# Kernel tuning notes

Hardware: AMD Instinct MI355X
Metric: run time of the kernel (lower is better)

Reference implementation:

```python
import jax, jax.numpy as jnp
import numpy as np

# Standard SMPL kinematic tree (24 joints); parents[0] = -1 (root)
PARENTS = np.array([-1, 0, 0, 0, 1, 2, 3, 4, 5, 6, 7, 8, 9, 9, 9, 12, 13, 14, 16, 17, 18, 19, 20, 21], dtype=np.int32)
B, V, J, NSHAPE, NPOSEBASIS = 512, 6890, 24, 10, 207


def setup_inputs() -> dict:
    key = jax.random.key(0)
    ks = jax.random.split(key, 9)
    poses = jax.random.normal(ks[0], (B, J * 3), dtype=jnp.float32) * 0.2
    shapes = jax.random.normal(ks[1], (B, NSHAPE), dtype=jnp.float32)
    Rh = jax.random.normal(ks[2], (B, 3), dtype=jnp.float32) * 0.2
    Th = jax.random.normal(ks[3], (B, 3), dtype=jnp.float32)
    v_template = jax.random.normal(ks[4], (V, 3), dtype=jnp.float32)
    shapedirs = jax.random.normal(ks[5], (V, 3, NSHAPE), dtype=jnp.float32) * 0.01
    posedirs = jax.random.normal(ks[6], (NPOSEBASIS, V * 3), dtype=jnp.float32) * 0.01
    jr = jax.random.uniform(ks[7], (J, V), dtype=jnp.float32)
    J_regressor = jr / jnp.sum(jr, axis=1, keepdims=True)
    w = jax.random.uniform(ks[8], (V, J), dtype=jnp.float32)
    weights = w / jnp.sum(w, axis=1, keepdims=True)
    return {"poses": poses, "shapes": shapes, "Rh": Rh, "Th": Th,
            "v_template": v_template, "shapedirs": shapedirs, "posedirs": posedirs,
            "J_regressor": J_regressor, "weights": weights}


def batch_rodrigues(rot_vecs):
    # rot_vecs: (N,3) -> (N,3,3); matches smplx batch_rodrigues
    angle = jnp.linalg.norm(rot_vecs + 1e-8, axis=1, keepdims=True)  # (N,1)
    rd = rot_vecs / angle
    cos = jnp.cos(angle)[:, :, None]
    sin = jnp.sin(angle)[:, :, None]
    rx, ry, rz = rd[:, 0], rd[:, 1], rd[:, 2]
    zeros = jnp.zeros_like(rx)
    K = jnp.stack([zeros, -rz, ry, rz, zeros, -rx, -ry, rx, zeros], axis=1).reshape(-1, 3, 3)
    ident = jnp.eye(3, dtype=rot_vecs.dtype)[None]
    return ident + sin * K + (1.0 - cos) * jnp.matmul(K, K)


def smpl_forward(poses, shapes, Rh, Th, v_template, shapedirs, posedirs, J_regressor, weights):
    bn = poses.shape[0]
    # shape blendshapes: v_shaped (B,V,3)
    v_shaped = v_template[None] + jnp.einsum('bl,vdl->bvd', shapes, shapedirs)
    # rest-pose joints (B,J,3)
    Jrest = jnp.einsum('jv,bvd->bjd', J_regressor, v_shaped)
    # per-joint rotation matrices
    rot_mats = batch_rodrigues(poses.reshape(-1, 3)).reshape(bn, J, 3, 3)
    # pose blendshapes
    ident = jnp.eye(3, dtype=poses.dtype)
    pose_feature = (rot_mats[:, 1:] - ident).reshape(bn, -1)  # (B,207)
    v_posed = v_shaped + jnp.matmul(pose_feature, posedirs).reshape(bn, V, 3)
    # kinematic chain rigid transforms
    rel_joints = jnp.concatenate([Jrest[:, :1], Jrest[:, 1:] - Jrest[:, PARENTS[1:]]], axis=1)
    bottom = jnp.tile(jnp.array([0., 0., 0., 1.], dtype=poses.dtype), (bn, J, 1, 1))
    tmats = jnp.concatenate([jnp.concatenate([rot_mats, rel_joints[..., None]], axis=-1), bottom], axis=-2)  # (B,J,4,4)
    chain = [tmats[:, 0]]
    for i in range(1, J):
        chain.append(jnp.matmul(chain[PARENTS[i]], tmats[:, i]))
    transforms = jnp.stack(chain, axis=1)  # (B,J,4,4)
    # remove rest-pose joint location from transforms
    tj = jnp.einsum('bjik,bjk->bji', transforms[:, :, :3, :3], Jrest)
    A = transforms.at[:, :, :3, 3].add(-tj)
    # linear blend skinning
    T = jnp.einsum('vj,bjik->bvik', weights, A)  # (B,V,4,4)
    verts = jnp.einsum('bvik,bvk->bvi', T[:, :, :3, :3], v_posed) + T[:, :, :3, 3]
    # global rotation + translation
    rot = batch_rodrigues(Rh)  # (B,3,3)
    vertices = jnp.einsum('bij,bvj->bvi', rot, verts) + Th[:, None]
    return vertices


def reference(poses, shapes, Rh, Th, v_template, shapedirs, posedirs, J_regressor, weights):
    return smpl_forward(poses, shapes, Rh, Th, v_template, shapedirs, posedirs, J_regressor, weights)
```

## Files before the change

kernel.cpp:

```cpp
#include <hip/hip_runtime.h>


#define BN 512
#define NV 6890
#define NVP 6912
#define NJ 24
#define NS 10
#define NP 207
#define PSTR 208
#define KP 224
#define K2 32
#define NPAD 20736
#define BB 8
#define TV 256

#define WS_JSP 0
#define WS_G   6400
#define WS_PF  153856
#define WS_A1  12800
#define WS_A2  127488
#define WS_WT  324096
#define WS_BT  545280
#define FULL_NEED ((size_t)10380288)
#define FB_NEED   ((size_t)1041408)

typedef unsigned short u16;
typedef short bf16x8 __attribute__((ext_vector_type(8)));
typedef float f32x4  __attribute__((ext_vector_type(4)));

__constant__ int c_par[NJ] = {-1,0,0,0,1,2,3,4,5,6,7,8,9,9,9,12,13,14,16,17,18,19,20,21};

__device__ __forceinline__ u16 f2bf(float f){
    union { float f; unsigned i; } x; x.f = f;
    unsigned r = x.i + 0x7fffu + ((x.i >> 16) & 1u);
    return (u16)(r >> 16);
}

__global__ __launch_bounds__(256) void k_jreg(const float* __restrict__ jreg,
                                              const float* __restrict__ vt,
                                              const float* __restrict__ sd,
                                              float* __restrict__ ws){
    int j = blockIdx.x, s = blockIdx.y;
    int tid = threadIdx.x;
    int v0 = s*864, v1 = min(NV, v0+864);
    float acc[33];
    #pragma unroll
    for(int k=0;k<33;k++) acc[k]=0.f;
    for(int v=v0+tid; v<v1; v+=256){
        float jr = jreg[j*NV+v];
        #pragma unroll
        for(int d=0;d<3;d++) acc[d] = fmaf(jr, vt[v*3+d], acc[d]);
        const float2* sp = (const float2*)(sd + (size_t)v*30);
        #pragma unroll
        for(int k=0;k<15;k++){
            float2 s2 = sp[k];
            acc[3+2*k]   = fmaf(jr, s2.x, acc[3+2*k]);
            acc[3+2*k+1] = fmaf(jr, s2.y, acc[3+2*k+1]);
        }
    }
    __shared__ float red[4][33];
    int lane = tid & 63, wv = tid >> 6;
    #pragma unroll
    for(int k=0;k<33;k++){
        float val = acc[k];
        #pragma unroll
        for(int off=32; off; off>>=1) val += __shfl_down(val, off, 64);
        if(lane==0) red[wv][k]=val;
    }
    __syncthreads();
    if(tid<33) ws[WS_JSP + (j*8+s)*33 + tid] = red[0][tid]+red[1][tid]+red[2][tid]+red[3][tid];
}

__global__ __launch_bounds__(256) void k_conv(const float* __restrict__ pd,
                                              const float* __restrict__ sd,
                                              u16* __restrict__ bt){
    __shared__ u16 tile[32][65];
    int t = threadIdx.x;
    int n0 = blockIdx.x * 64;
    int k0 = blockIdx.y * 32;
    int nl = t & 63, kb = (t>>6)*8;
    int n = n0 + nl;
    #pragma unroll
    for(int i=0;i<8;i++){
        int k = k0 + kb + i;
        float v = 0.f;
        if(n < NV*3){
            if(k < NP)           v = pd[(size_t)k*(NV*3) + n];
            else if(k < NP+NS)   v = sd[(size_t)(n/3)*30 + (n%3)*10 + (k-NP)];
        }
        tile[kb+i][nl] = f2bf(v);
    }
    __syncthreads();
    int nl2 = t >> 2, kc = t & 3;
    union { u16 s[8]; uint4 q; } u;
    #pragma unroll
    for(int i=0;i<8;i++) u.s[i] = tile[kc*8+i][nl2];
    int ng = n0 + nl2;
    int row = (ng%3)*NVP + ng/3;
    u16* dst = bt + (size_t)row*KP + k0 + kc*8;
    *(uint4*)dst = u.q;
}

__global__ __launch_bounds__(256) void k_wconv(const float* __restrict__ wts,
                                               u16* __restrict__ wt){
    int v = blockIdx.x*256 + threadIdx.x;
    if(v >= NVP) return;
    union { u16 s[32]; uint4 q[4]; } u;
    #pragma unroll
    for(int j=0;j<24;j++) u.s[j] = (v<NV) ? f2bf(wts[(size_t)v*24+j]) : (u16)0;
    #pragma unroll
    for(int j=24;j<32;j++) u.s[j]=0;
    uint4* dst = (uint4*)(wt + (size_t)v*K2);
    dst[0]=u.q[0]; dst[1]=u.q[1]; dst[2]=u.q[2]; dst[3]=u.q[3];
}

__global__ __launch_bounds__(64) void k_chain(const float* __restrict__ poses,
                                              const float* __restrict__ shapes,
                                              const float* __restrict__ Rh,
                                              float* __restrict__ ws,
                                              u16* __restrict__ a1,
                                              u16* __restrict__ a2,
                                              int full){
    int b = blockIdx.x;
    int t = threadIdx.x;
    __shared__ float R[25][9];
    __shared__ float sh[NS];
    __shared__ float js[792];
    __shared__ float jrest[NJ][3];
    __shared__ float rel[NJ][3];
    __shared__ float chR[NJ][9];
    __shared__ float chT[NJ][3];
    __shared__ float Gs[NJ][12];

    if(t<25){
        float x,y,z;
        if(t<24){ x=poses[b*72+t*3]; y=poses[b*72+t*3+1]; z=poses[b*72+t*3+2]; }
        else    { x=Rh[b*3];         y=Rh[b*3+1];         z=Rh[b*3+2]; }
        float ax=x+1e-8f, ay=y+1e-8f, az=z+1e-8f;
        float ang = sqrtf(ax*ax+ay*ay+az*az);
        float inv = 1.f/ang;
        float rx=x*inv, ry=y*inv, rz=z*inv;
        float s = sinf(ang), c = cosf(ang), oc = 1.f - c;
        R[t][0]=1.f+oc*(-rz*rz-ry*ry); R[t][1]=-s*rz+oc*(rx*ry);      R[t][2]= s*ry+oc*(rx*rz);
        R[t][3]= s*rz+oc*(rx*ry);      R[t][4]=1.f+oc*(-rz*rz-rx*rx); R[t][5]=-s*rx+oc*(ry*rz);
        R[t][6]=-s*ry+oc*(rx*rz);      R[t][7]= s*rx+oc*(ry*rz);      R[t][8]=1.f+oc*(-ry*ry-rx*rx);
    }
    if(t<NS) sh[t]=shapes[b*NS+t];
    for(int idx=t; idx<792; idx+=64){
        int j = idx/33, e = idx%33;
        float a = 0.f;
        #pragma unroll
        for(int s=0;s<8;s++) a += ws[WS_JSP + (j*8+s)*33 + e];
        js[idx]=a;
    }
    __syncthreads();

    for(int idx=t; idx<KP; idx+=64){
        float v = 0.f;
        if(idx<NP){
            int j = 1 + idx/9, e = idx%9;
            v = R[j][e] - ((e==0||e==4||e==8)?1.f:0.f);
        } else if(idx<NP+NS) v = sh[idx-NP];
        if(full){ a1[b*KP + idx] = f2bf(v); }
        else if(idx<PSTR) ws[WS_PF + b*PSTR + idx] = (idx<NP)?v:0.f;
    }
    if(t<NJ){
        #pragma unroll
        for(int d=0;d<3;d++){
            float a = js[t*33 + d];
            #pragma unroll
            for(int l=0;l<NS;l++) a = fmaf(sh[l], js[t*33 + 3 + d*10 + l], a);
            jrest[t][d]=a;
        }
    }
    __syncthreads();
    if(t<NJ){
        int p = c_par[t];
        #pragma unroll
        for(int d=0;d<3;d++) rel[t][d] = (t==0) ? jrest[0][d] : jrest[t][d]-jrest[p][d];
    }
    __syncthreads();
    if(t<9) chR[0][t]=R[0][t];
    if(t<3) chT[0][t]=rel[0][t];
    __syncthreads();
    for(int i=1;i<NJ;i++){
        if(t<12){
            int r=t>>2, cc=t&3, p=c_par[i];
            if(cc<3){
                chR[i][r*3+cc] = chR[p][r*3+0]*R[i][0*3+cc] + chR[p][r*3+1]*R[i][1*3+cc] + chR[p][r*3+2]*R[i][2*3+cc];
            } else {
                chT[i][r] = chR[p][r*3+0]*rel[i][0] + chR[p][r*3+1]*rel[i][1] + chR[p][r*3+2]*rel[i][2] + chT[p][r];
            }
        }
        __syncthreads();
    }
    if(t<NJ){
        float rg[9];
        #pragma unroll
        for(int k=0;k<9;k++) rg[k]=R[24][k];
        float at[3];
        #pragma unroll
        for(int r=0;r<3;r++){
            float tj = chR[t][r*3+0]*jrest[t][0] + chR[t][r*3+1]*jrest[t][1] + chR[t][r*3+2]*jrest[t][2];
            at[r] = chT[t][r] - tj;
        }
        #pragma unroll
        for(int r=0;r<3;r++){
            #pragma unroll
            for(int cc=0;cc<3;cc++)
                Gs[t][r*4+cc] = rg[r*3+0]*chR[t][0*3+cc] + rg[r*3+1]*chR[t][1*3+cc] + rg[r*3+2]*chR[t][2*3+cc];
            Gs[t][r*4+3] = rg[r*3+0]*at[0] + rg[r*3+1]*at[1] + rg[r*3+2]*at[2];
        }
    }
    __syncthreads();
    if(full){
        for(int idx=t; idx<12*K2; idx+=64){
            int e = idx/K2, k = idx%K2;
            float v = (k<NJ) ? Gs[k][e] : 0.f;
            a2[((size_t)e*BN + b)*K2 + k] = f2bf(v);
        }
    } else if(t<NJ){
        float* g = &ws[WS_G + b*288 + t*12];
        #pragma unroll
        for(int e=0;e<12;e++) g[e] = Gs[t][e];
    }
}

__global__ __launch_bounds__(256) void k_fused(const u16* __restrict__ A1,
                                               const u16* __restrict__ A2,
                                               const u16* __restrict__ WT,
                                               const u16* __restrict__ BT,
                                               const float* __restrict__ vt,
                                               const float* __restrict__ th,
                                               float* __restrict__ out){
    int t = threadIdx.x;
    int wave = t>>6, lane = t&63;
    int quad = lane>>4, l16 = lane&15;
    int m0 = blockIdx.x*32 + (wave&1)*16;
    int v0 = blockIdx.y*32 + (wave>>1)*16;
    f32x4 zz = {0.f,0.f,0.f,0.f};
    f32x4 accP[3]; accP[0]=zz; accP[1]=zz; accP[2]=zz;
    f32x4 accT[12];
    #pragma unroll
    for(int e=0;e<12;e++) accT[e]=zz;

    const u16* a1 = A1 + (size_t)(m0 + l16)*KP + quad*8;
    const u16* b0 = BT + ((size_t)0*NVP + v0 + l16)*KP + quad*8;
    const u16* b1 = BT + ((size_t)1*NVP + v0 + l16)*KP + quad*8;
    const u16* b2 = BT + ((size_t)2*NVP + v0 + l16)*KP + quad*8;
    #pragma unroll
    for(int k0=0;k0<KP;k0+=32){
        bf16x8 af = *(const bf16x8*)(a1 + k0);
        bf16x8 f0 = *(const bf16x8*)(b0 + k0);
        bf16x8 f1 = *(const bf16x8*)(b1 + k0);
        bf16x8 f2 = *(const bf16x8*)(b2 + k0);
        accP[0] = __builtin_amdgcn_mfma_f32_16x16x32_bf16(af, f0, accP[0], 0,0,0);
        accP[1] = __builtin_amdgcn_mfma_f32_16x16x32_bf16(af, f1, accP[1], 0,0,0);
        accP[2] = __builtin_amdgcn_mfma_f32_16x16x32_bf16(af, f2, accP[2], 0,0,0);
    }
    bf16x8 wf = *(const bf16x8*)(WT + (size_t)(v0 + l16)*K2 + quad*8);
    #pragma unroll
    for(int e=0;e<12;e++){
        bf16x8 gf = *(const bf16x8*)(A2 + ((size_t)e*BN + m0 + l16)*K2 + quad*8);
        accT[e] = __builtin_amdgcn_mfma_f32_16x16x32_bf16(gf, wf, accT[e], 0,0,0);
    }
    int v = v0 + l16;
    if(v < NV){
        float vt0 = vt[v*3], vt1 = vt[v*3+1], vt2 = vt[v*3+2];
        #pragma unroll
        for(int r=0;r<4;r++){
            int b = m0 + quad*4 + r;
            float p0 = accP[0][r] + vt0;
            float p1 = accP[1][r] + vt1;
            float p2 = accP[2][r] + vt2;
            float o0 = fmaf(accT[0][r],p0, fmaf(accT[1][r],p1, fmaf(accT[2][r], p2, accT[3][r]))) + th[b*3+0];
            float o1 = fmaf(accT[4][r],p0, fmaf(accT[5][r],p1, fmaf(accT[6][r], p2, accT[7][r]))) + th[b*3+1];
            float o2 = fmaf(accT[8][r],p0, fmaf(accT[9][r],p1, fmaf(accT[10][r],p2, accT[11][r]))) + th[b*3+2];
            float* op = out + ((size_t)b*NV + v)*3;
            op[0]=o0; op[1]=o1; op[2]=o2;
        }
    }
}

__global__ __launch_bounds__(256) void k_main(const float* __restrict__ vt,
                                              const float* __restrict__ sd,
                                              const float* __restrict__ pd,
                                              const float* __restrict__ wts,
                                              const float* __restrict__ th,
                                              const float* __restrict__ shapes,
                                              const float* __restrict__ ws,
                                              float* __restrict__ out){
    __shared__ __align__(16) float pf_s[BB*PSTR];
    __shared__ __align__(16) float g_s[BB*288];
    __shared__ float th_s[BB*3];
    __shared__ float sh_s[BB*NS];
    int tid = threadIdx.x;
    int b0  = blockIdx.y * BB;
    int v   = blockIdx.x * TV + tid;

    for(int i=tid; i<BB*PSTR; i+=TV) pf_s[i] = ws[WS_PF + b0*PSTR + i];
    for(int i=tid; i<BB*288;  i+=TV) g_s[i]  = ws[WS_G  + b0*288  + i];
    if(tid<BB*3)  th_s[tid] = th[b0*3+tid];
    if(tid<BB*NS) sh_s[tid] = shapes[b0*NS+tid];
    __syncthreads();
    if(v>=NV) return;

    float sdv[30];
    {
        const float2* sp = (const float2*)(sd + (size_t)v*30);
        #pragma unroll
        for(int i=0;i<15;i++){ float2 s2 = sp[i]; sdv[2*i]=s2.x; sdv[2*i+1]=s2.y; }
    }
    float vt0=vt[v*3], vt1=vt[v*3+1], vt2=vt[v*3+2];
    float vp[BB][3];
    #pragma unroll
    for(int b=0;b<BB;b++){
        #pragma unroll
        for(int d=0;d<3;d++){
            float a = (d==0)?vt0:((d==1)?vt1:vt2);
            #pragma unroll
            for(int l=0;l<NS;l++) a = fmaf(sh_s[b*NS+l], sdv[d*10+l], a);
            vp[b][d]=a;
        }
    }
    const float* pcol = pd + (size_t)v*3;
    int p=0;
    for(; p<=NP-4; p+=4){
        float pdv[4][3];
        #pragma unroll
        for(int q=0;q<4;q++){
            size_t base = (size_t)(p+q)*(NV*3);
            pdv[q][0]=pcol[base]; pdv[q][1]=pcol[base+1]; pdv[q][2]=pcol[base+2];
        }
        #pragma unroll
        for(int b=0;b<BB;b++){
            float4 f = *(const float4*)&pf_s[b*PSTR+p];
            #pragma unroll
            for(int d=0;d<3;d++)
                vp[b][d] = fmaf(f.x,pdv[0][d], fmaf(f.y,pdv[1][d], fmaf(f.z,pdv[2][d], fmaf(f.w,pdv[3][d], vp[b][d]))));
        }
    }
    for(; p<NP; p++){
        size_t base=(size_t)p*(NV*3);
        float p0=pcol[base], p1=pcol[base+1], p2=pcol[base+2];
        #pragma unroll
        for(int b=0;b<BB;b++){
            float f = pf_s[b*PSTR+p];
            vp[b][0]=fmaf(f,p0,vp[b][0]); vp[b][1]=fmaf(f,p1,vp[b][1]); vp[b][2]=fmaf(f,p2,vp[b][2]);
        }
    }
    float w[24];
    {
        const float4* wp = (const float4*)(wts + (size_t)v*24);
        #pragma unroll
        for(int i=0;i<6;i++){
            float4 u = wp[i];
            w[i*4+0]=u.x; w[i*4+1]=u.y; w[i*4+2]=u.z; w[i*4+3]=u.w;
        }
    }
    #pragma unroll 1
    for(int b=0;b<BB;b++){
        float4 T0=make_float4(0.f,0.f,0.f,0.f), T1=T0, T2=T0;
        #pragma unroll
        for(int j=0;j<NJ;j++){
            float wj = w[j];
            const float4* g = (const float4*)&g_s[b*288 + j*12];
            float4 g0=g[0], g1=g[1], g2=g[2];
            T0.x=fmaf(wj,g0.x,T0.x); T0.y=fmaf(wj,g0.y,T0.y); T0.z=fmaf(wj,g0.z,T0.z); T0.w=fmaf(wj,g0.w,T0.w);
            T1.x=fmaf(wj,g1.x,T1.x); T1.y=fmaf(wj,g1.y,T1.y); T1.z=fmaf(wj,g1.z,T1.z); T1.w=fmaf(wj,g1.w,T1.w);
            T2.x=fmaf(wj,g2.x,T2.x); T2.y=fmaf(wj,g2.y,T2.y); T2.z=fmaf(wj,g2.z,T2.z); T2.w=fmaf(wj,g2.w,T2.w);
        }
        float x=vp[b][0], y=vp[b][1], z=vp[b][2];
        float ox = fmaf(T0.x,x, fmaf(T0.y,y, fmaf(T0.z,z, T0.w))) + th_s[b*3+0];
        float oy = fmaf(T1.x,x, fmaf(T1.y,y, fmaf(T1.z,z, T1.w))) + th_s[b*3+1];
        float oz = fmaf(T2.x,x, fmaf(T2.y,y, fmaf(T2.z,z, T2.w))) + th_s[b*3+2];
        size_t o = ((size_t)(b0+b)*NV + v)*3;
        out[o]=ox; out[o+1]=oy; out[o+2]=oz;
    }
}

extern "C" void kernel_launch(void* const* d_in, const int* in_sizes, int n_in,
                              void* d_out, int out_size, void* d_ws, size_t ws_size,
                              hipStream_t stream){
    const float* poses  = (const float*)d_in[0];
    const float* shapes = (const float*)d_in[1];
    const float* Rh     = (const float*)d_in[2];
    const float* Th     = (const float*)d_in[3];
    const float* vt     = (const float*)d_in[4];
    const float* sd     = (const float*)d_in[5];
    const float* pdirs  = (const float*)d_in[6];
    const float* jreg   = (const float*)d_in[7];
    const float* wts    = (const float*)d_in[8];
    float* ws  = (float*)d_ws;
    float* out = (float*)d_out;
    u16* u = (u16*)d_ws;
    int full = (ws_size >= FULL_NEED) ? 1 : 0;

    hipLaunchKernelGGL(k_jreg, dim3(NJ,8), dim3(256), 0, stream, jreg, vt, sd, ws);
    hipLaunchKernelGGL(k_chain, dim3(BN), dim3(64), 0, stream, poses, shapes, Rh, ws,
                       u + WS_A1, u + WS_A2, full);
    if(full){
        hipLaunchKernelGGL(k_conv, dim3(NPAD/64, KP/32), dim3(256), 0, stream,
                           pdirs, sd, u + WS_BT);
        hipLaunchKernelGGL(k_wconv, dim3(NVP/256), dim3(256), 0, stream, wts, u + WS_WT);
        hipLaunchKernelGGL(k_fused, dim3(BN/32, NVP/32), dim3(256), 0, stream,
                           u + WS_A1, u + WS_A2, u + WS_WT, u + WS_BT, vt, Th, out);
    } else {
        hipLaunchKernelGGL(k_main, dim3((NV+TV-1)/TV, BN/BB), dim3(256), 0, stream,
                           vt, sd, pdirs, wts, Th, shapes, ws, out);
    }
}
```

Baseline: 164.1 us.

## Keep vertex B-fragments in registers and loop over batch tiles with coalesced chunked layout

Changes the bf16 operand layouts to a chunk-major form (8-element chunks strided by row count), so each lane's 16-byte fragment loads are contiguous across lanes. The fused kernel now has each wave own 16 vertices, load all 21 posedir/shapedir fragments once into registers, and loop over four 16-row batch tiles. This reuses the large B operand across more batch rows and enlarges the block tile to 64x64. The cost is higher register pressure, which may lower occupancy, and the batch loads are repeated per mi iteration.

```diff
diff --git a/kernel.cpp b/kernel.cpp
--- a/kernel.cpp
+++ b/kernel.cpp
@@ -9,7 +9,6 @@
 #define NP 207
 #define PSTR 208
 #define KP 224
-#define K2 32
 #define NPAD 20736
 #define BB 8
 #define TV 256
@@ -22,7 +21,6 @@
 #define WS_WT  324096
 #define WS_BT  545280
 #define FULL_NEED ((size_t)10380288)
-#define FB_NEED   ((size_t)1041408)
 
 typedef unsigned short u16;
 typedef short bf16x8 __attribute__((ext_vector_type(8)));
@@ -96,9 +94,9 @@
     #pragma unroll
     for(int i=0;i<8;i++) u.s[i] = tile[kc*8+i][nl2];
     int ng = n0 + nl2;
-    int row = (ng%3)*NVP + ng/3;
-    u16* dst = bt + (size_t)row*KP + k0 + kc*8;
-    *(uint4*)dst = u.q;
+    int v = ng/3, d = ng%3;
+    int chunk = (k0>>3) + kc;
+    *(uint4*)(bt + (((size_t)d*28 + chunk)*NVP + v)*8) = u.q;
 }
 
 __global__ __launch_bounds__(256) void k_wconv(const float* __restrict__ wts,
@@ -110,8 +108,9 @@
     for(int j=0;j<24;j++) u.s[j] = (v<NV) ? f2bf(wts[(size_t)v*24+j]) : (u16)0;
     #pragma unroll
     for(int j=24;j<32;j++) u.s[j]=0;
-    uint4* dst = (uint4*)(wt + (size_t)v*K2);
-    dst[0]=u.q[0]; dst[1]=u.q[1]; dst[2]=u.q[2]; dst[3]=u.q[3];
+    #pragma unroll
+    for(int c=0;c<4;c++)
+        *(uint4*)(wt + ((size_t)c*NVP + v)*8) = u.q[c];
 }
 
 __global__ __launch_bounds__(64) void k_chain(const float* __restrict__ poses,
@@ -161,7 +160,7 @@
             int j = 1 + idx/9, e = idx%9;
             v = R[j][e] - ((e==0||e==4||e==8)?1.f:0.f);
         } else if(idx<NP+NS) v = sh[idx-NP];
-        if(full){ a1[b*KP + idx] = f2bf(v); }
+        if(full){ a1[(((size_t)(idx>>3))*BN + b)*8 + (idx&7)] = f2bf(v); }
         else if(idx<PSTR) ws[WS_PF + b*PSTR + idx] = (idx<NP)?v:0.f;
     }
     if(t<NJ){
@@ -214,10 +213,10 @@
     }
     __syncthreads();
     if(full){
-        for(int idx=t; idx<12*K2; idx+=64){
-            int e = idx/K2, k = idx%K2;
+        for(int idx=t; idx<12*32; idx+=64){
+            int e = idx>>5, k = idx&31;
             float v = (k<NJ) ? Gs[k][e] : 0.f;
-            a2[((size_t)e*BN + b)*K2 + k] = f2bf(v);
+            a2[((((size_t)e*4)+(k>>3))*BN + b)*8 + (k&7)] = f2bf(v);
         }
     } else if(t<NJ){
         float* g = &ws[WS_G + b*288 + t*12];
@@ -234,50 +233,53 @@
                                                const float* __restrict__ th,
                                                float* __restrict__ out){
     int t = threadIdx.x;
-    int wave = t>>6, lane = t&63;
+    int w = t>>6, lane = t&63;
     int quad = lane>>4, l16 = lane&15;
-    int m0 = blockIdx.x*32 + (wave&1)*16;
-    int v0 = blockIdx.y*32 + (wave>>1)*16;
+    int v = blockIdx.y*64 + w*16 + l16;
+
+    bf16x8 Bf[3][7];
+    #pragma unroll
+    for(int d=0;d<3;d++)
+        #pragma unroll
+        for(int s=0;s<7;s++)
+            Bf[d][s] = *(const bf16x8*)(BT + (((size_t)d*28 + s*4 + quad)*NVP + v)*8);
+    bf16x8 wf = *(const bf16x8*)(WT + ((size_t)quad*NVP + v)*8);
+    float vt0=0.f, vt1=0.f, vt2=0.f;
+    if(v<NV){ vt0=vt[v*3]; vt1=vt[v*3+1]; vt2=vt[v*3+2]; }
     f32x4 zz = {0.f,0.f,0.f,0.f};
-    f32x4 accP[3]; accP[0]=zz; accP[1]=zz; accP[2]=zz;
-    f32x4 accT[12];
-    #pragma unroll
-    for(int e=0;e<12;e++) accT[e]=zz;
-
-    const u16* a1 = A1 + (size_t)(m0 + l16)*KP + quad*8;
-    const u16* b0 = BT + ((size_t)0*NVP + v0 + l16)*KP + quad*8;
-    const u16* b1 = BT + ((size_t)1*NVP + v0 + l16)*KP + quad*8;
-    const u16* b2 = BT + ((size_t)2*NVP + v0 + l16)*KP + quad*8;
-    #pragma unroll
-    for(int k0=0;k0<KP;k0+=32){
-        bf16x8 af = *(const bf16x8*)(a1 + k0);
-        bf16x8 f0 = *(const bf16x8*)(b0 + k0);
-        bf16x8 f1 = *(const bf16x8*)(b1 + k0);
-        bf16x8 f2 = *(const bf16x8*)(b2 + k0);
-        accP[0] = __builtin_amdgcn_mfma_f32_16x16x32_bf16(af, f0, accP[0], 0,0,0);
-        accP[1] = __builtin_amdgcn_mfma_f32_16x16x32_bf16(af, f1, accP[1], 0,0,0);
-        accP[2] = __builtin_amdgcn_mfma_f32_16x16x32_bf16(af, f2, accP[2], 0,0,0);
-    }
-    bf16x8 wf = *(const bf16x8*)(WT + (size_t)(v0 + l16)*K2 + quad*8);
-    #pragma unroll
-    for(int e=0;e<12;e++){
-        bf16x8 gf = *(const bf16x8*)(A2 + ((size_t)e*BN + m0 + l16)*K2 + quad*8);
-        accT[e] = __builtin_amdgcn_mfma_f32_16x16x32_bf16(gf, wf, accT[e], 0,0,0);
-    }
-    int v = v0 + l16;
-    if(v < NV){
-        float vt0 = vt[v*3], vt1 = vt[v*3+1], vt2 = vt[v*3+2];
-        #pragma unroll
-        for(int r=0;r<4;r++){
-            int b = m0 + quad*4 + r;
-            float p0 = accP[0][r] + vt0;
-            float p1 = accP[1][r] + vt1;
-            float p2 = accP[2][r] + vt2;
-            float o0 = fmaf(accT[0][r],p0, fmaf(accT[1][r],p1, fmaf(accT[2][r], p2, accT[3][r]))) + th[b*3+0];
-            float o1 = fmaf(accT[4][r],p0, fmaf(accT[5][r],p1, fmaf(accT[6][r], p2, accT[7][r]))) + th[b*3+1];
-            float o2 = fmaf(accT[8][r],p0, fmaf(accT[9][r],p1, fmaf(accT[10][r],p2, accT[11][r]))) + th[b*3+2];
-            float* op = out + ((size_t)b*NV + v)*3;
-            op[0]=o0; op[1]=o1; op[2]=o2;
+
+    #pragma unroll
+    for(int mi=0;mi<4;mi++){
+        int m0 = blockIdx.x*64 + mi*16;
+        int mrow = m0 + l16;
+        f32x4 accP0=zz, accP1=zz, accP2=zz;
+        #pragma unroll
+        for(int s=0;s<7;s++){
+            bf16x8 af = *(const bf16x8*)(A1 + (((size_t)s*4 + quad)*BN + mrow)*8);
+            accP0 = __builtin_amdgcn_mfma_f32_16x16x32_bf16(af, Bf[0][s], accP0, 0,0,0);
+            accP1 = __builtin_amdgcn_mfma_f32_16x16x32_bf16(af, Bf[1][s], accP1, 0,0,0);
+            accP2 = __builtin_amdgcn_mfma_f32_16x16x32_bf16(af, Bf[2][s], accP2, 0,0,0);
+        }
+        f32x4 accT[12];
+        #pragma unroll
+        for(int e=0;e<12;e++){
+            bf16x8 gf = *(const bf16x8*)(A2 + (((size_t)e*4 + quad)*BN + mrow)*8);
+            accT[e] = __builtin_amdgcn_mfma_f32_16x16x32_bf16(gf, wf, zz, 0,0,0);
+        }
+        if(v < NV){
+            #pragma unroll
+            for(int r=0;r<4;r++){
+                int b = m0 + quad*4 + r;
+                float t0 = th[b*3+0], t1 = th[b*3+1], t2 = th[b*3+2];
+                float p0 = accP0[r] + vt0;
+                float p1 = accP1[r] + vt1;
+                float p2 = accP2[r] + vt2;
+                float o0 = fmaf(accT[0][r],p0, fmaf(accT[1][r],p1, fmaf(accT[2][r], p2, accT[3][r]))) + t0;
+                float o1 = fmaf(accT[4][r],p0, fmaf(accT[5][r],p1, fmaf(accT[6][r], p2, accT[7][r]))) + t1;
+                float o2 = fmaf(accT[8][r],p0, fmaf(accT[9][r],p1, fmaf(accT[10][r],p2, accT[11][r]))) + t2;
+                float* op = out + ((size_t)b*NV + v)*3;
+                op[0]=o0; op[1]=o1; op[2]=o2;
+            }
         }
     }
 }
@@ -403,7 +405,7 @@
         hipLaunchKernelGGL(k_conv, dim3(NPAD/64, KP/32), dim3(256), 0, stream,
                            pdirs, sd, u + WS_BT);
         hipLaunchKernelGGL(k_wconv, dim3(NVP/256), dim3(256), 0, stream, wts, u + WS_WT);
-        hipLaunchKernelGGL(k_fused, dim3(BN/32, NVP/32), dim3(256), 0, stream,
+        hipLaunchKernelGGL(k_fused, dim3(BN/64, NVP/64), dim3(256), 0, stream,
                            u + WS_A1, u + WS_A2, u + WS_WT, u + WS_BT, vt, Th, out);
     } else {
         hipLaunchKernelGGL(k_main, dim3((NV+TV-1)/TV, BN/BB), dim3(256), 0, stream,
```

Measured after the change: 157.4 us. 4.1% less time.
